# Performance work log

Measured on AMD Instinct MI355X. Metric: run time of the kernel, lower is better.

## Reference

```python
import jax, jax.numpy as jnp
import numpy as np

N, E = 1024, 128
NEG_SLOPE = 0.2


def lrelu(x):
    return jnp.where(x >= 0, x, NEG_SLOPE * x)


def setup_inputs() -> dict:
    key = jax.random.key(0)
    ks = jax.random.split(key, 8)
    embs = jax.random.normal(ks[0], (N, E), jnp.float32)
    # 0/1 adjacency; force self-loops so every softmax row has >=1 valid entry
    adj = jax.random.randint(ks[1], (N, N), 0, 2).astype(jnp.int32)
    adj = adj.at[jnp.arange(N), jnp.arange(N)].set(1)
    pde = jax.random.normal(ks[2], (N, N, E), jnp.float32)
    # learned params; linear weights stored as (in, out) so y = x @ W + b
    s1 = 1.0 / np.sqrt(E)      # self.w: Linear(E, E, bias=False)
    W = jax.random.uniform(ks[3], (E, E), jnp.float32, -s1, s1)
    s2 = 1.0 / np.sqrt(2 * E)  # self.pc: Linear(2E, E); self.a: Linear(2E, 1)
    pc_W = jax.random.uniform(ks[4], (2 * E, E), jnp.float32, -s2, s2)
    pc_b = jax.random.uniform(ks[5], (E,), jnp.float32, -s2, s2)
    a_W = jax.random.uniform(ks[6], (2 * E,), jnp.float32, -s2, s2)
    a_b = jax.random.uniform(ks[7], (), jnp.float32, -s2, s2)
    return {"embs": embs, "adj": adj, "pde": pde, "W": W,
            "pc_W": pc_W, "pc_b": pc_b, "a_W": a_W, "a_b": a_b}


def reference(embs, adj, pde, W, pc_W, pc_b, a_W, a_b):
    # wf = self.w(embs)                                   [N, E]
    wf = embs @ W
    # pc = lrelu(self.pc(cat([cm, pde], -1)))             [N, N, E]
    # cm[i, j] = wf[j]; split pc_W to avoid materializing cat([cm, pde])
    pc_Wc, pc_Wp = pc_W[:E], pc_W[E:]
    c_term = wf @ pc_Wc                                   # [N, E], broadcast over rows i
    pc = lrelu(c_term[None, :, :] + jnp.einsum('ijk,kl->ijl', pde, pc_Wp) + pc_b)
    # pc = self.w(pc)                                     [N, N, E]
    pc = jnp.einsum('ijk,kl->ijl', pc, W)
    # mf = lrelu(self.a(cat([rm, pc], -1))); rm[i, j] = wf[i]
    a1, a2 = a_W[:E], a_W[E:]
    logits = lrelu((wf @ a1)[:, None] + jnp.einsum('ijk,k->ij', pc, a2) + a_b)  # [N, N]
    # masked softmax over dim=1: adj==1 -> 0, adj==0 -> -inf (nan_to_num semantics)
    mask = jnp.where(adj == 1, 0.0, -jnp.inf)
    attn = jax.nn.softmax(logits + mask, axis=1)
    nbc = attn @ embs                                     # [N, E]
    return jnp.concatenate([embs, nbc], axis=1)           # [N, 2E]
```

## Files before the change

### kernel.cpp

```cpp
#include <hip/hip_runtime.h>
#include <hip/hip_bf16.h>

#define N 1024
#define E 128
#define NEG 0.2f
#define AST 136

typedef __attribute__((ext_vector_type(8))) short short8;
typedef __attribute__((ext_vector_type(4))) float float4v;

__device__ __forceinline__ short f2bf(float x){
  unsigned u = __float_as_uint(x);
  u += 0x7fffu + ((u >> 16) & 1u);
  return (short)(u >> 16);
}

__device__ __forceinline__ short8 cvt8(const float* __restrict__ p){
  float4 a = *(const float4*)p;
  float4 b = *(const float4*)(p + 4);
  short8 r;
  r[0] = f2bf(a.x); r[1] = f2bf(a.y); r[2] = f2bf(a.z); r[3] = f2bf(a.w);
  r[4] = f2bf(b.x); r[5] = f2bf(b.y); r[6] = f2bf(b.z); r[7] = f2bf(b.w);
  return r;
}

__global__ void prep0(const float* __restrict__ W, const float* __restrict__ pc_W,
                      const float* __restrict__ a_W, short* __restrict__ BT,
                      float* __restrict__ w2){
  int l = blockIdx.x, t = threadIdx.x;
  BT[l*E + t] = f2bf(pc_W[(E + t)*E + l]);
  __shared__ float red[E];
  red[t] = W[l*E + t] * a_W[E + t];
  __syncthreads();
  for (int s = 64; s > 0; s >>= 1){ if (t < s) red[t] += red[t+s]; __syncthreads(); }
  if (t == 0) w2[l] = red[0];
}

__global__ void prep1(const float* __restrict__ embs, const float* __restrict__ W,
                      const float* __restrict__ pc_W, const float* __restrict__ pc_b,
                      const float* __restrict__ a_W,
                      float* __restrict__ bias, float* __restrict__ u){
  int j = blockIdx.x, t = threadIdx.x;
  __shared__ float se[E], swf[E], red[E];
  se[t] = embs[j*E + t];
  __syncthreads();
  float acc = 0.f;
  #pragma unroll 8
  for (int k = 0; k < E; k++) acc += se[k] * W[k*E + t];
  swf[t] = acc;
  __syncthreads();
  float ct = 0.f;
  #pragma unroll 8
  for (int k = 0; k < E; k++) ct += swf[k] * pc_W[k*E + t];
  bias[j*E + t] = ct + pc_b[t];
  red[t] = swf[t] * a_W[t];
  __syncthreads();
  for (int s = 64; s > 0; s >>= 1){ if (t < s) red[t] += red[t+s]; __syncthreads(); }
  if (t == 0) u[j] = red[0];
}

__global__ __launch_bounds__(256, 3)
void main_gemm(const float* __restrict__ pde, const short* __restrict__ BT,
               const float* __restrict__ bias, const float* __restrict__ u,
               const float* __restrict__ w2, const float* __restrict__ a_b,
               float* __restrict__ logits){
  __shared__ short sB[E*AST];
  __shared__ float sBias[E], sW2[E], sU[128];
  const int t = threadIdx.x;
  const int j = blockIdx.x, it = blockIdx.y;
  const int i0 = it * 128;

  {
    int rl = t >> 4;
    int kk = (t & 15) * 8;
    #pragma unroll
    for (int p = 0; p < 8; p++){
      int l = p*16 + rl;
      *(uint4*)(&sB[l*AST + kk]) = *(const uint4*)(&BT[l*E + kk]);
    }
  }
  if (t < 128){
    sBias[t] = bias[j*E + t];
    sW2[t]   = w2[t];
    sU[t]    = u[i0 + t];
  }

  const int lane = t & 63;
  const int w = t >> 6;
  const int n = lane & 15;
  const int q = lane >> 4;
  const int rw = w * 32;

  short8 afrag[2][4];
  #pragma unroll
  for (int mt = 0; mt < 2; mt++){
    int m = rw + mt*16 + n;
    const float* rowp = pde + ((size_t)(i0 + m) * N + j) * E;
    #pragma unroll
    for (int ks = 0; ks < 4; ks++)
      afrag[mt][ks] = cvt8(rowp + ks*32 + q*8);
  }

  __syncthreads();

  float4v acc[2][8];
  #pragma unroll
  for (int mt = 0; mt < 2; mt++)
    #pragma unroll
    for (int ct = 0; ct < 8; ct++)
      acc[mt][ct] = (float4v){0.f, 0.f, 0.f, 0.f};

  #pragma unroll
  for (int ks = 0; ks < 4; ks++){
    int ko = ks*32 + q*8;
    #pragma unroll
    for (int ct = 0; ct < 8; ct++){
      short8 b = *(const short8*)(&sB[(ct*16 + n)*AST + ko]);
      acc[0][ct] = __builtin_amdgcn_mfma_f32_16x16x32_bf16(afrag[0][ks], b, acc[0][ct], 0, 0, 0);
      acc[1][ct] = __builtin_amdgcn_mfma_f32_16x16x32_bf16(afrag[1][ks], b, acc[1][ct], 0, 0, 0);
    }
  }

  const float ab = a_b[0];
  #pragma unroll
  for (int mt = 0; mt < 2; mt++){
    #pragma unroll
    for (int r = 0; r < 4; r++){
      float s = 0.f;
      #pragma unroll
      for (int ct = 0; ct < 8; ct++){
        int l = ct*16 + n;
        float y = acc[mt][ct][r] + sBias[l];
        y = (y >= 0.f) ? y : NEG * y;
        s += y * sW2[l];
      }
      s += __shfl_xor(s, 1, 64);
      s += __shfl_xor(s, 2, 64);
      s += __shfl_xor(s, 4, 64);
      s += __shfl_xor(s, 8, 64);
      if (n == 0){
        int m = rw + mt*16 + q*4 + r;
        float lg = sU[m] + s + ab;
        lg = (lg >= 0.f) ? lg : NEG * lg;
        logits[(size_t)(i0 + m) * N + j] = lg;
      }
    }
  }
}

__global__ __launch_bounds__(256)
void softmax_nbc(const float* __restrict__ logits, const int* __restrict__ adj,
                 const float* __restrict__ embs, float* __restrict__ out){
  __shared__ float sAttn[N];
  __shared__ float wred[4];
  __shared__ float red[256];
  int i = blockIdx.x, t = threadIdx.x;
  int lane = t & 63, wv = t >> 6;
  float mymax = -__builtin_inff();
  #pragma unroll
  for (int p = 0; p < 4; p++){
    int j = p*256 + t;
    float v = logits[(size_t)i*N + j];
    v = (adj[(size_t)i*N + j] == 1) ? v : -__builtin_inff();
    sAttn[j] = v;
    mymax = fmaxf(mymax, v);
  }
  #pragma unroll
  for (int o = 32; o > 0; o >>= 1) mymax = fmaxf(mymax, __shfl_xor(mymax, o, 64));
  if (lane == 0) wred[wv] = mymax;
  __syncthreads();
  float M = fmaxf(fmaxf(wred[0], wred[1]), fmaxf(wred[2], wred[3]));
  __syncthreads();
  float mysum = 0.f;
  #pragma unroll
  for (int p = 0; p < 4; p++){
    int j = p*256 + t;
    float e = __expf(sAttn[j] - M);
    sAttn[j] = e;
    mysum += e;
  }
  #pragma unroll
  for (int o = 32; o > 0; o >>= 1) mysum += __shfl_xor(mysum, o, 64);
  if (lane == 0) wred[wv] = mysum;
  __syncthreads();
  float inv = 1.0f / (wred[0] + wred[1] + wred[2] + wred[3]);
  __syncthreads();
  int l = t & 127, jh = t >> 7;
  float acc = 0.f;
  #pragma unroll 8
  for (int jj = 0; jj < 512; jj++){
    int j = jh*512 + jj;
    acc += sAttn[j] * embs[j*E + l];
  }
  red[t] = acc; __syncthreads();
  if (t < 128){
    out[(size_t)i*2*E + t]     = embs[i*E + t];
    out[(size_t)i*2*E + E + t] = (red[t] + red[t+128]) * inv;
  }
}

extern "C" void kernel_launch(void* const* d_in, const int* in_sizes, int n_in,
                              void* d_out, int out_size, void* d_ws, size_t ws_size,
                              hipStream_t stream) {
  const float* embs = (const float*)d_in[0];
  const int*   adj  = (const int*)d_in[1];
  const float* pde  = (const float*)d_in[2];
  const float* W    = (const float*)d_in[3];
  const float* pc_W = (const float*)d_in[4];
  const float* pc_b = (const float*)d_in[5];
  const float* a_W  = (const float*)d_in[6];
  const float* a_b  = (const float*)d_in[7];
  float* out = (float*)d_out;

  float* ws      = (float*)d_ws;
  float* logits  = ws;
  float* bias    = ws + (size_t)N*N;
  float* u       = bias + (size_t)N*E;
  float* w2      = u + N;
  short* BT      = (short*)(w2 + E);

  prep0<<<dim3(E), dim3(E), 0, stream>>>(W, pc_W, a_W, BT, w2);
  prep1<<<dim3(N), dim3(E), 0, stream>>>(embs, W, pc_W, pc_b, a_W, bias, u);
  main_gemm<<<dim3(N, N/128), dim3(256), 0, stream>>>(pde, BT, bias, u, w2, a_b, logits);
  softmax_nbc<<<dim3(N), dim3(256), 0, stream>>>(logits, adj, embs, out);
}
```

Baseline: 758.6 us.

## Process several j columns per block with register-prefetched pde loads

Each main_gemm block now handles JB=8 consecutive j values rather than one. The LDS load of the transposed weight tile BT is spread over eight GEMMs instead of one, and the pde fp32 data for the next j is loaded into registers while the current j's MFMAs run. The grid shrinks eightfold and occupancy is capped at 2 blocks per SIMD because the prefetch buffers raise register pressure. This is meant to hide global memory latency on the 512MB pde stream.

```diff
diff --git a/kernel.cpp b/kernel.cpp
--- a/kernel.cpp
+++ b/kernel.cpp
@@ -5,6 +5,7 @@
 #define E 128
 #define NEG 0.2f
 #define AST 136
+#define JB 8
 
 typedef __attribute__((ext_vector_type(8))) short short8;
 typedef __attribute__((ext_vector_type(4))) float float4v;
@@ -15,9 +16,7 @@
   return (short)(u >> 16);
 }
 
-__device__ __forceinline__ short8 cvt8(const float* __restrict__ p){
-  float4 a = *(const float4*)p;
-  float4 b = *(const float4*)(p + 4);
+__device__ __forceinline__ short8 cvt2(float4 a, float4 b){
   short8 r;
   r[0] = f2bf(a.x); r[1] = f2bf(a.y); r[2] = f2bf(a.z); r[3] = f2bf(a.w);
   r[4] = f2bf(b.x); r[5] = f2bf(b.y); r[6] = f2bf(b.z); r[7] = f2bf(b.w);
@@ -59,16 +58,17 @@
   if (t == 0) u[j] = red[0];
 }
 
-__global__ __launch_bounds__(256, 3)
+__global__ __launch_bounds__(256, 2)
 void main_gemm(const float* __restrict__ pde, const short* __restrict__ BT,
                const float* __restrict__ bias, const float* __restrict__ u,
                const float* __restrict__ w2, const float* __restrict__ a_b,
                float* __restrict__ logits){
   __shared__ short sB[E*AST];
-  __shared__ float sBias[E], sW2[E], sU[128];
+  __shared__ float sBias[JB][E];
+  __shared__ float sW2[E], sU[128];
   const int t = threadIdx.x;
-  const int j = blockIdx.x, it = blockIdx.y;
-  const int i0 = it * 128;
+  const int jg = blockIdx.x, it = blockIdx.y;
+  const int j0 = jg * JB, i0 = it * 128;
 
   {
     int rl = t >> 4;
@@ -79,11 +79,12 @@
       *(uint4*)(&sB[l*AST + kk]) = *(const uint4*)(&BT[l*E + kk]);
     }
   }
-  if (t < 128){
-    sBias[t] = bias[j*E + t];
-    sW2[t]   = w2[t];
-    sU[t]    = u[i0 + t];
-  }
+  #pragma unroll
+  for (int p = 0; p < JB*E/256; p++){
+    int idx = p*256 + t;
+    sBias[idx >> 7][idx & 127] = bias[(size_t)(j0 + (idx >> 7))*E + (idx & 127)];
+  }
+  if (t < 128){ sW2[t] = w2[t]; sU[t] = u[i0 + t]; }
 
   const int lane = t & 63;
   const int w = t >> 6;
@@ -91,58 +92,82 @@
   const int q = lane >> 4;
   const int rw = w * 32;
 
-  short8 afrag[2][4];
-  #pragma unroll
-  for (int mt = 0; mt < 2; mt++){
-    int m = rw + mt*16 + n;
-    const float* rowp = pde + ((size_t)(i0 + m) * N + j) * E;
-    #pragma unroll
-    for (int ks = 0; ks < 4; ks++)
-      afrag[mt][ks] = cvt8(rowp + ks*32 + q*8);
-  }
-
-  __syncthreads();
-
-  float4v acc[2][8];
-  #pragma unroll
-  for (int mt = 0; mt < 2; mt++)
-    #pragma unroll
-    for (int ct = 0; ct < 8; ct++)
-      acc[mt][ct] = (float4v){0.f, 0.f, 0.f, 0.f};
-
+  const float* rp0 = pde + ((size_t)(i0 + rw + n)      * N + j0) * E + q*8;
+  const float* rp1 = pde + ((size_t)(i0 + rw + 16 + n) * N + j0) * E + q*8;
+
+  float4 raw[2][4][2];
   #pragma unroll
   for (int ks = 0; ks < 4; ks++){
-    int ko = ks*32 + q*8;
-    #pragma unroll
-    for (int ct = 0; ct < 8; ct++){
-      short8 b = *(const short8*)(&sB[(ct*16 + n)*AST + ko]);
-      acc[0][ct] = __builtin_amdgcn_mfma_f32_16x16x32_bf16(afrag[0][ks], b, acc[0][ct], 0, 0, 0);
-      acc[1][ct] = __builtin_amdgcn_mfma_f32_16x16x32_bf16(afrag[1][ks], b, acc[1][ct], 0, 0, 0);
-    }
-  }
+    raw[0][ks][0] = *(const float4*)(rp0 + ks*32);
+    raw[0][ks][1] = *(const float4*)(rp0 + ks*32 + 4);
+    raw[1][ks][0] = *(const float4*)(rp1 + ks*32);
+    raw[1][ks][1] = *(const float4*)(rp1 + ks*32 + 4);
+  }
+
+  __syncthreads();
 
   const float ab = a_b[0];
-  #pragma unroll
-  for (int mt = 0; mt < 2; mt++){
-    #pragma unroll
-    for (int r = 0; r < 4; r++){
-      float s = 0.f;
+
+  #pragma unroll 2
+  for (int jj = 0; jj < JB; jj++){
+    short8 frag[2][4];
+    #pragma unroll
+    for (int mt = 0; mt < 2; mt++)
+      #pragma unroll
+      for (int ks = 0; ks < 4; ks++)
+        frag[mt][ks] = cvt2(raw[mt][ks][0], raw[mt][ks][1]);
+
+    if (jj < JB-1){
+      int off = (jj+1) * E;
+      #pragma unroll
+      for (int ks = 0; ks < 4; ks++){
+        raw[0][ks][0] = *(const float4*)(rp0 + off + ks*32);
+        raw[0][ks][1] = *(const float4*)(rp0 + off + ks*32 + 4);
+        raw[1][ks][0] = *(const float4*)(rp1 + off + ks*32);
+        raw[1][ks][1] = *(const float4*)(rp1 + off + ks*32 + 4);
+      }
+    }
+
+    float4v acc[2][8];
+    #pragma unroll
+    for (int mt = 0; mt < 2; mt++)
+      #pragma unroll
+      for (int ct = 0; ct < 8; ct++)
+        acc[mt][ct] = (float4v){0.f, 0.f, 0.f, 0.f};
+
+    #pragma unroll
+    for (int ks = 0; ks < 4; ks++){
+      int ko = ks*32 + q*8;
       #pragma unroll
       for (int ct = 0; ct < 8; ct++){
-        int l = ct*16 + n;
-        float y = acc[mt][ct][r] + sBias[l];
-        y = (y >= 0.f) ? y : NEG * y;
-        s += y * sW2[l];
+        short8 b = *(const short8*)(&sB[(ct*16 + n)*AST + ko]);
+        acc[0][ct] = __builtin_amdgcn_mfma_f32_16x16x32_bf16(frag[0][ks], b, acc[0][ct], 0, 0, 0);
+        acc[1][ct] = __builtin_amdgcn_mfma_f32_16x16x32_bf16(frag[1][ks], b, acc[1][ct], 0, 0, 0);
       }
-      s += __shfl_xor(s, 1, 64);
-      s += __shfl_xor(s, 2, 64);
-      s += __shfl_xor(s, 4, 64);
-      s += __shfl_xor(s, 8, 64);
-      if (n == 0){
-        int m = rw + mt*16 + q*4 + r;
-        float lg = sU[m] + s + ab;
-        lg = (lg >= 0.f) ? lg : NEG * lg;
-        logits[(size_t)(i0 + m) * N + j] = lg;
+    }
+
+    #pragma unroll
+    for (int mt = 0; mt < 2; mt++){
+      #pragma unroll
+      for (int r = 0; r < 4; r++){
+        float s = 0.f;
+        #pragma unroll
+        for (int ct = 0; ct < 8; ct++){
+          int l = ct*16 + n;
+          float y = acc[mt][ct][r] + sBias[jj][l];
+          y = (y >= 0.f) ? y : NEG * y;
+          s += y * sW2[l];
+        }
+        s += __shfl_xor(s, 1, 64);
+        s += __shfl_xor(s, 2, 64);
+        s += __shfl_xor(s, 4, 64);
+        s += __shfl_xor(s, 8, 64);
+        if (n == 0){
+          int m = rw + mt*16 + q*4 + r;
+          float lg = sU[m] + s + ab;
+          lg = (lg >= 0.f) ? lg : NEG * lg;
+          logits[(size_t)(i0 + m) * N + j0 + jj] = lg;
+        }
       }
     }
   }
@@ -221,6 +246,6 @@
 
   prep0<<<dim3(E), dim3(E), 0, stream>>>(W, pc_W, a_W, BT, w2);
   prep1<<<dim3(N), dim3(E), 0, stream>>>(embs, W, pc_W, pc_b, a_W, bias, u);
-  main_gemm<<<dim3(N, N/128), dim3(256), 0, stream>>>(pde, BT, bias, u, w2, a_b, logits);
+  main_gemm<<<dim3(N/JB, N/128), dim3(256), 0, stream>>>(pde, BT, bias, u, w2, a_b, logits);
   softmax_nbc<<<dim3(N), dim3(256), 0, stream>>>(logits, adj, embs, out);
 }
```

New measurement: 862.6 us. 13.7% more time.

## Cut main GEMM register use by per-column-tile epilogue, merge prep kernels, vectorize softmax

Applied to the files above, without the earlier changes.

The main GEMM now computes each 16-column tile's accumulators and immediately applies bias, leaky-ReLU and the w2 dot product, so it holds two accumulators instead of sixteen. This is meant to allow raising launch bounds from 3 to 4 blocks per SIMD and so keep more pde loads in flight. The two prep kernels are merged into one launch to save launch overhead. The softmax kernel now uses vectorized float4/int4 loads and keeps values in registers, dropping one LDS round trip and one barrier. The main risk is that the pde-bandwidth-bound GEMM changes little, and forcing 4 waves may cause register spills.

```diff
diff --git a/kernel.cpp b/kernel.cpp
--- a/kernel.cpp
+++ b/kernel.cpp
@@ -15,51 +15,48 @@
   return (short)(u >> 16);
 }
 
-__device__ __forceinline__ short8 cvt8(const float* __restrict__ p){
-  float4 a = *(const float4*)p;
-  float4 b = *(const float4*)(p + 4);
+__device__ __forceinline__ short8 cvt2(float4 a, float4 b){
   short8 r;
   r[0] = f2bf(a.x); r[1] = f2bf(a.y); r[2] = f2bf(a.z); r[3] = f2bf(a.w);
   r[4] = f2bf(b.x); r[5] = f2bf(b.y); r[6] = f2bf(b.z); r[7] = f2bf(b.w);
   return r;
 }
 
-__global__ void prep0(const float* __restrict__ W, const float* __restrict__ pc_W,
-                      const float* __restrict__ a_W, short* __restrict__ BT,
-                      float* __restrict__ w2){
-  int l = blockIdx.x, t = threadIdx.x;
-  BT[l*E + t] = f2bf(pc_W[(E + t)*E + l]);
-  __shared__ float red[E];
-  red[t] = W[l*E + t] * a_W[E + t];
-  __syncthreads();
-  for (int s = 64; s > 0; s >>= 1){ if (t < s) red[t] += red[t+s]; __syncthreads(); }
-  if (t == 0) w2[l] = red[0];
-}
-
-__global__ void prep1(const float* __restrict__ embs, const float* __restrict__ W,
-                      const float* __restrict__ pc_W, const float* __restrict__ pc_b,
-                      const float* __restrict__ a_W,
-                      float* __restrict__ bias, float* __restrict__ u){
-  int j = blockIdx.x, t = threadIdx.x;
+__global__ void prep(const float* __restrict__ embs, const float* __restrict__ W,
+                     const float* __restrict__ pc_W, const float* __restrict__ pc_b,
+                     const float* __restrict__ a_W,
+                     short* __restrict__ BT, float* __restrict__ w2,
+                     float* __restrict__ bias, float* __restrict__ u){
+  int b = blockIdx.x, t = threadIdx.x;
   __shared__ float se[E], swf[E], red[E];
-  se[t] = embs[j*E + t];
-  __syncthreads();
-  float acc = 0.f;
-  #pragma unroll 8
-  for (int k = 0; k < E; k++) acc += se[k] * W[k*E + t];
-  swf[t] = acc;
-  __syncthreads();
-  float ct = 0.f;
-  #pragma unroll 8
-  for (int k = 0; k < E; k++) ct += swf[k] * pc_W[k*E + t];
-  bias[j*E + t] = ct + pc_b[t];
-  red[t] = swf[t] * a_W[t];
-  __syncthreads();
-  for (int s = 64; s > 0; s >>= 1){ if (t < s) red[t] += red[t+s]; __syncthreads(); }
-  if (t == 0) u[j] = red[0];
-}
-
-__global__ __launch_bounds__(256, 3)
+  if (b < E){
+    int l = b;
+    BT[l*E + t] = f2bf(pc_W[(E + t)*E + l]);
+    red[t] = W[l*E + t] * a_W[E + t];
+    __syncthreads();
+    for (int s = 64; s > 0; s >>= 1){ if (t < s) red[t] += red[t+s]; __syncthreads(); }
+    if (t == 0) w2[l] = red[0];
+  } else {
+    int j = b - E;
+    se[t] = embs[j*E + t];
+    __syncthreads();
+    float acc = 0.f;
+    #pragma unroll 8
+    for (int k = 0; k < E; k++) acc += se[k] * W[k*E + t];
+    swf[t] = acc;
+    __syncthreads();
+    float ct = 0.f;
+    #pragma unroll 8
+    for (int k = 0; k < E; k++) ct += swf[k] * pc_W[k*E + t];
+    bias[j*E + t] = ct + pc_b[t];
+    red[t] = swf[t] * a_W[t];
+    __syncthreads();
+    for (int s = 64; s > 0; s >>= 1){ if (t < s) red[t] += red[t+s]; __syncthreads(); }
+    if (t == 0) u[j] = red[0];
+  }
+}
+
+__global__ __launch_bounds__(256, 4)
 void main_gemm(const float* __restrict__ pde, const short* __restrict__ BT,
                const float* __restrict__ bias, const float* __restrict__ u,
                const float* __restrict__ w2, const float* __restrict__ a_b,
@@ -91,59 +88,68 @@
   const int q = lane >> 4;
   const int rw = w * 32;
 
-  short8 afrag[2][4];
-  #pragma unroll
-  for (int mt = 0; mt < 2; mt++){
-    int m = rw + mt*16 + n;
-    const float* rowp = pde + ((size_t)(i0 + m) * N + j) * E;
+  const float* rp0 = pde + ((size_t)(i0 + rw + n)      * N + j) * E + q*8;
+  const float* rp1 = pde + ((size_t)(i0 + rw + 16 + n) * N + j) * E + q*8;
+
+  short8 frag[2][4];
+  #pragma unroll
+  for (int ks = 0; ks < 4; ks++){
+    float4 a0 = *(const float4*)(rp0 + ks*32);
+    float4 a1 = *(const float4*)(rp0 + ks*32 + 4);
+    float4 b0 = *(const float4*)(rp1 + ks*32);
+    float4 b1 = *(const float4*)(rp1 + ks*32 + 4);
+    frag[0][ks] = cvt2(a0, a1);
+    frag[1][ks] = cvt2(b0, b1);
+  }
+
+  __syncthreads();
+
+  const float ab = a_b[0];
+  float s0[4] = {0.f, 0.f, 0.f, 0.f};
+  float s1[4] = {0.f, 0.f, 0.f, 0.f};
+
+  #pragma unroll
+  for (int ct = 0; ct < 8; ct++){
+    const int l = ct*16 + n;
+    short8 b[4];
     #pragma unroll
     for (int ks = 0; ks < 4; ks++)
-      afrag[mt][ks] = cvt8(rowp + ks*32 + q*8);
-  }
-
-  __syncthreads();
-
-  float4v acc[2][8];
-  #pragma unroll
-  for (int mt = 0; mt < 2; mt++)
-    #pragma unroll
-    for (int ct = 0; ct < 8; ct++)
-      acc[mt][ct] = (float4v){0.f, 0.f, 0.f, 0.f};
-
-  #pragma unroll
-  for (int ks = 0; ks < 4; ks++){
-    int ko = ks*32 + q*8;
-    #pragma unroll
-    for (int ct = 0; ct < 8; ct++){
-      short8 b = *(const short8*)(&sB[(ct*16 + n)*AST + ko]);
-      acc[0][ct] = __builtin_amdgcn_mfma_f32_16x16x32_bf16(afrag[0][ks], b, acc[0][ct], 0, 0, 0);
-      acc[1][ct] = __builtin_amdgcn_mfma_f32_16x16x32_bf16(afrag[1][ks], b, acc[1][ct], 0, 0, 0);
-    }
-  }
-
-  const float ab = a_b[0];
-  #pragma unroll
-  for (int mt = 0; mt < 2; mt++){
+      b[ks] = *(const short8*)(&sB[l*AST + ks*32 + q*8]);
+
+    float4v acc0 = (float4v){0.f,0.f,0.f,0.f};
+    float4v acc1 = (float4v){0.f,0.f,0.f,0.f};
+    #pragma unroll
+    for (int ks = 0; ks < 4; ks++){
+      acc0 = __builtin_amdgcn_mfma_f32_16x16x32_bf16(frag[0][ks], b[ks], acc0, 0, 0, 0);
+      acc1 = __builtin_amdgcn_mfma_f32_16x16x32_bf16(frag[1][ks], b[ks], acc1, 0, 0, 0);
+    }
+
+    const float bl = sBias[l], wl = sW2[l];
     #pragma unroll
     for (int r = 0; r < 4; r++){
-      float s = 0.f;
-      #pragma unroll
-      for (int ct = 0; ct < 8; ct++){
-        int l = ct*16 + n;
-        float y = acc[mt][ct][r] + sBias[l];
-        y = (y >= 0.f) ? y : NEG * y;
-        s += y * sW2[l];
-      }
-      s += __shfl_xor(s, 1, 64);
-      s += __shfl_xor(s, 2, 64);
-      s += __shfl_xor(s, 4, 64);
-      s += __shfl_xor(s, 8, 64);
-      if (n == 0){
-        int m = rw + mt*16 + q*4 + r;
-        float lg = sU[m] + s + ab;
-        lg = (lg >= 0.f) ? lg : NEG * lg;
-        logits[(size_t)(i0 + m) * N + j] = lg;
-      }
+      float y0 = acc0[r] + bl; y0 = (y0 >= 0.f) ? y0 : NEG * y0;
+      float y1 = acc1[r] + bl; y1 = (y1 >= 0.f) ? y1 : NEG * y1;
+      s0[r] += y0 * wl;
+      s1[r] += y1 * wl;
+    }
+  }
+
+  #pragma unroll
+  for (int r = 0; r < 4; r++){
+    float a = s0[r], c = s1[r];
+    a += __shfl_xor(a, 1, 64); c += __shfl_xor(c, 1, 64);
+    a += __shfl_xor(a, 2, 64); c += __shfl_xor(c, 2, 64);
+    a += __shfl_xor(a, 4, 64); c += __shfl_xor(c, 4, 64);
+    a += __shfl_xor(a, 8, 64); c += __shfl_xor(c, 8, 64);
+    if (n == 0){
+      int m0 = rw + q*4 + r;
+      float lg = sU[m0] + a + ab;
+      lg = (lg >= 0.f) ? lg : NEG * lg;
+      logits[(size_t)(i0 + m0) * N + j] = lg;
+      int m1 = rw + 16 + q*4 + r;
+      float lh = sU[m1] + c + ab;
+      lh = (lh >= 0.f) ? lh : NEG * lh;
+      logits[(size_t)(i0 + m1) * N + j] = lh;
     }
   }
 }
@@ -156,35 +162,30 @@
   __shared__ float red[256];
   int i = blockIdx.x, t = threadIdx.x;
   int lane = t & 63, wv = t >> 6;
-  float mymax = -__builtin_inff();
-  #pragma unroll
-  for (int p = 0; p < 4; p++){
-    int j = p*256 + t;
-    float v = logits[(size_t)i*N + j];
-    v = (adj[(size_t)i*N + j] == 1) ? v : -__builtin_inff();
-    sAttn[j] = v;
-    mymax = fmaxf(mymax, v);
-  }
+
+  float4 lv = *(const float4*)(logits + (size_t)i*N + 4*t);
+  int4   av = *(const int4*)  (adj    + (size_t)i*N + 4*t);
+  float v0 = (av.x == 1) ? lv.x : -__builtin_inff();
+  float v1 = (av.y == 1) ? lv.y : -__builtin_inff();
+  float v2 = (av.z == 1) ? lv.z : -__builtin_inff();
+  float v3 = (av.w == 1) ? lv.w : -__builtin_inff();
+  float mymax = fmaxf(fmaxf(v0, v1), fmaxf(v2, v3));
   #pragma unroll
   for (int o = 32; o > 0; o >>= 1) mymax = fmaxf(mymax, __shfl_xor(mymax, o, 64));
   if (lane == 0) wred[wv] = mymax;
   __syncthreads();
   float M = fmaxf(fmaxf(wred[0], wred[1]), fmaxf(wred[2], wred[3]));
   __syncthreads();
-  float mysum = 0.f;
-  #pragma unroll
-  for (int p = 0; p < 4; p++){
-    int j = p*256 + t;
-    float e = __expf(sAttn[j] - M);
-    sAttn[j] = e;
-    mysum += e;
-  }
+
+  float e0 = __expf(v0 - M), e1 = __expf(v1 - M), e2 = __expf(v2 - M), e3 = __expf(v3 - M);
+  *(float4*)(&sAttn[4*t]) = (float4){e0, e1, e2, e3};
+  float mysum = (e0 + e1) + (e2 + e3);
   #pragma unroll
   for (int o = 32; o > 0; o >>= 1) mysum += __shfl_xor(mysum, o, 64);
   if (lane == 0) wred[wv] = mysum;
   __syncthreads();
   float inv = 1.0f / (wred[0] + wred[1] + wred[2] + wred[3]);
-  __syncthreads();
+
   int l = t & 127, jh = t >> 7;
   float acc = 0.f;
   #pragma unroll 8
@@ -219,8 +220,7 @@
   float* w2      = u + N;
   short* BT      = (short*)(w2 + E);
 
-  prep0<<<dim3(E), dim3(E), 0, stream>>>(W, pc_W, a_W, BT, w2);
-  prep1<<<dim3(N), dim3(E), 0, stream>>>(embs, W, pc_W, pc_b, a_W, bias, u);
+  prep<<<dim3(E + N), dim3(E), 0, stream>>>(embs, W, pc_W, pc_b, a_W, BT, w2, bias, u);
   main_gemm<<<dim3(N, N/128), dim3(256), 0, stream>>>(pde, BT, bias, u, w2, a_b, logits);
   softmax_nbc<<<dim3(N), dim3(256), 0, stream>>>(logits, adj, embs, out);
 }
```

New measurement: 744.2 us. Within noise of the previous version (-1.9%).
